# Performance work log

Measured on AMD Instinct MI355X. Metric: run time of the kernel, lower is better.

## Reference

```python
import jax, jax.numpy as jnp
import numpy as np

DIM = 128
EXPAND = 2
INTERNAL = DIM * EXPAND  # 256
MAX_SEQ = 2048
BATCH = 32
GATE_DECAY = 3.0


def _gated_cell(x, Wa, ba, Wi, bi, g):
    # x: [B,S,D]; Wa,Wi: [E,D]; ba,bi,g: [E]
    pa = jnp.einsum('bsd,ed->bse', x, Wa) + ba          # projected activation
    pi = jnp.einsum('bsd,ed->bse', x, Wi) + bi          # projected input
    reset_gate = jax.nn.sigmoid(pa)
    input_gate = jax.nn.sigmoid(pi)
    alpha = jax.nn.sigmoid(g)                           # [E]
    a = alpha / jnp.power(GATE_DECAY, reset_gate)       # adaptive alpha [B,S,E]
    u = jnp.sqrt(1.0 - a * a) * (input_gate * pi)       # per-step input [B,S,E]

    def step(h, au):
        a_t, u_t = au
        h = a_t * h + u_t
        return h, h

    h0 = jnp.zeros((x.shape[0], Wa.shape[0]), x.dtype)
    _, ys = jax.lax.scan(step, h0, (a.transpose(1, 0, 2), u.transpose(1, 0, 2)))
    return ys.transpose(1, 0, 2)                        # [B,S,E]


def _recency_weights(seq_len, dtype):
    w = jnp.exp(jnp.linspace(0.0, 3.0, MAX_SEQ))[:seq_len]
    return w.astype(dtype).reshape(1, -1, 1)


def setup_inputs() -> dict:
    key = jax.random.key(0)
    ks = jax.random.split(key, 12)
    std = 1.0 / np.sqrt(DIM)  # kaiming fan_in linear
    lo = float(np.log(0.9 / 0.1))
    hi = float(np.log(0.999 / 0.001))
    d = {
        'x': jax.random.normal(ks[0], (BATCH, MAX_SEQ, DIM), jnp.float32),
        'Wa_u': jax.random.normal(ks[1], (INTERNAL, DIM), jnp.float32) * std,
        'ba_u': jnp.zeros((INTERNAL,), jnp.float32),
        'Wi_u': jax.random.normal(ks[2], (INTERNAL, DIM), jnp.float32) * std,
        'bi_u': jnp.zeros((INTERNAL,), jnp.float32),
        'g_u': jax.random.uniform(ks[3], (INTERNAL,), jnp.float32, lo, hi),
        'Wa_w': jax.random.normal(ks[4], (INTERNAL, DIM), jnp.float32) * std,
        'ba_w': jnp.zeros((INTERNAL,), jnp.float32),
        'Wi_w': jax.random.normal(ks[5], (INTERNAL, DIM), jnp.float32) * std,
        'bi_w': jnp.zeros((INTERNAL,), jnp.float32),
        'g_w': jax.random.uniform(ks[6], (INTERNAL,), jnp.float32, lo, hi),
        'Wf': jax.random.normal(ks[7], (DIM, 4 * DIM), jnp.float32) * (1.0 / np.sqrt(4 * DIM)),
        'bf': jnp.zeros((DIM,), jnp.float32),
    }
    return d


def reference(x, Wa_u, ba_u, Wi_u, bi_u, g_u, Wa_w, ba_w, Wi_w, bi_w, g_w, Wf, bf):
    unweighted = _gated_cell(x, Wa_u, ba_u, Wi_u, bi_u, g_u)          # [B,S,2D]
    xw = x * _recency_weights(x.shape[1], x.dtype)
    weighted = _gated_cell(xw, Wa_w, ba_w, Wi_w, bi_w, g_w)           # [B,S,2D]
    combined = jnp.concatenate([unweighted, weighted], axis=-1)       # [B,S,4D]
    return jnp.einsum('bsf,df->bsd', combined, Wf) + bf               # [B,S,D]
```

## Files before the change

kernel.cpp:

```cpp
#include <hip/hip_runtime.h>
#include <hip/hip_fp16.h>
#include <cstddef>
#include <cstdint>

#define DIM 128
#define SEQ 2048
#define NB 32
#define NCH 512
#define NROWS (NB * SEQ)

typedef _Float16 half8 __attribute__((ext_vector_type(8)));
typedef float    f32x4 __attribute__((ext_vector_type(4)));

#define CMB_BYTES ((size_t)NROWS * NCH * 2)
#define WFG_OFF   CMB_BYTES
#define WFG_BYTES ((size_t)NCH * DIM * 2)
#define WS_NEEDED (WFG_OFF + WFG_BYTES)

__device__ __forceinline__ float sigf(float v) {
    return __builtin_amdgcn_rcpf(1.0f + __builtin_amdgcn_exp2f(v * -1.44269504f));
}

__device__ __forceinline__ half8 cvt8(float4 v0, float4 v1) {
    auto p0 = __builtin_amdgcn_cvt_pkrtz(v0.x, v0.y);
    auto p1 = __builtin_amdgcn_cvt_pkrtz(v0.z, v0.w);
    auto p2 = __builtin_amdgcn_cvt_pkrtz(v1.x, v1.y);
    auto p3 = __builtin_amdgcn_cvt_pkrtz(v1.z, v1.w);
    union U { half8 h8; decltype(p0) p[4]; } u;
    u.p[0] = p0; u.p[1] = p1; u.p[2] = p2; u.p[3] = p3;
    return u.h8;
}

__global__ void k0_wfg(const float* __restrict__ Wf, _Float16* __restrict__ Wfg) {
    int t = blockIdx.x * 256 + threadIdx.x;
#pragma unroll
    for (int i = 0; i < 8; ++i) {
        int o = t * 8 + i;
        int j    = o & 7;
        int lane = (o >> 3) & 63;
        int q    = lane >> 4, n16 = lane & 15;
        int ct   = (o >> 9) & 7;
        int ks   = (o >> 12) & 1;
        int kb   = o >> 13;
        int k = kb * 64 + ks * 32 + q * 8 + j;
        int n = ct * 16 + n16;
        Wfg[o] = (_Float16)Wf[n * NCH + k];
    }
}

__global__ __launch_bounds__(512, 2) void kfused(
        const float* __restrict__ x,
        const float* __restrict__ Wa_u, const float* __restrict__ ba_u,
        const float* __restrict__ Wi_u, const float* __restrict__ bi_u,
        const float* __restrict__ g_u,
        const float* __restrict__ Wa_w, const float* __restrict__ ba_w,
        const float* __restrict__ Wi_w, const float* __restrict__ bi_w,
        const float* __restrict__ g_w,
        _Float16* __restrict__ cmb) {
    __shared__ _Float16 Bs[8192];
    __shared__ float2   seg[32][33];
    __shared__ float    pref[32][33];
    __shared__ float    carry[32];

    const int tid  = threadIdx.x;
    const int lane = tid & 63;
    const int w    = tid >> 6;
    const int quad = lane >> 4;
    const int n16  = lane & 15;

    const int b  = blockIdx.x;
    const int cg = blockIdx.y;
    const int p  = cg >> 3;
    const int ebase = (cg & 7) * 32;

    const float* Wa  = p ? Wa_w : Wa_u;
    const float* Wi  = p ? Wi_w : Wi_u;
    const float* bap = p ? ba_w : ba_u;
    const float* bip = p ? bi_w : bi_u;
    const float* gp  = p ? g_w  : g_u;

    for (int sl = tid; sl < 1024; sl += 512) {
        int l  = sl & 63;
        int nt = (sl >> 6) & 3;
        int ks = sl >> 8;
        int qq = l >> 4, nn = l & 15;
        int e = ebase + (nt & 1) * 16 + nn;
        const float* Wp = (nt >> 1) ? Wi : Wa;
        const float* src = Wp + (size_t)e * DIM + ks * 32 + qq * 8;
        float4 v0 = *(const float4*)src;
        float4 v1 = *(const float4*)(src + 4);
        *(half8*)&Bs[sl * 8] = cvt8(v0, v1);
    }

    float rba[2], rbi[2], ral[2];
#pragma unroll
    for (int hh = 0; hh < 2; ++hh) {
        int e = ebase + hh * 16 + n16;
        rba[hh] = bap[e];
        rbi[hh] = bip[e];
        ral[hh] = sigf(gp[e]);
    }
    if (tid < 32) carry[tid] = 0.0f;

    float scb = __expf((float)(w * 16 + quad * 4) * (3.0f / 2047.0f));
    const float r1    = __expf(3.0f / 2047.0f);
    const float r2    = r1 * r1;
    const float r3    = r2 * r1;
    const float cs128 = __expf(128.0f * 3.0f / 2047.0f);

    const float* xbase = x + ((size_t)b * SEQ + (size_t)(w * 16 + n16)) * DIM + quad * 8;
    _Float16* cmbb = cmb + (size_t)b * SEQ * NCH + cg * 32 + n16;

    __syncthreads();

    half8 af[4];
    {
        float4 xf0[8];
#pragma unroll
        for (int ks = 0; ks < 4; ++ks) {
            xf0[2 * ks]     = *(const float4*)(xbase + ks * 32);
            xf0[2 * ks + 1] = *(const float4*)(xbase + ks * 32 + 4);
        }
#pragma unroll
        for (int ks = 0; ks < 4; ++ks)
            af[ks] = cvt8(xf0[2 * ks], xf0[2 * ks + 1]);
    }

    for (int t = 0; t < 16; ++t) {
        const int s0 = t * 128;

        f32x4 acc[4];
#pragma unroll
        for (int nt = 0; nt < 4; ++nt) acc[nt] = (f32x4){0.f, 0.f, 0.f, 0.f};
#pragma unroll
        for (int ks = 0; ks < 4; ++ks) {
            half8 a = af[ks];
#pragma unroll
            for (int nt = 0; nt < 4; ++nt) {
                half8 bb = *(const half8*)&Bs[(ks * 256 + nt * 64 + lane) * 8];
                acc[nt] = __builtin_amdgcn_mfma_f32_16x16x32_f16(a, bb, acc[nt], 0, 0, 0);
            }
        }

        float4 xf[8];
        {
            int tn = (t + 1) & 15;
            const float* ab = xbase + (size_t)tn * 128 * DIM;
#pragma unroll
            for (int ks = 0; ks < 4; ++ks) {
                xf[2 * ks]     = *(const float4*)(ab + ks * 32);
                xf[2 * ks + 1] = *(const float4*)(ab + ks * 32 + 4);
            }
        }

        float sc[4];
        if (p) { sc[0] = scb; sc[1] = scb * r1; sc[2] = scb * r2; sc[3] = scb * r3; }
        else   { sc[0] = sc[1] = sc[2] = sc[3] = 1.0f; }
        scb *= cs128;

        float a_s[2][4], u_s[2][4];
#pragma unroll
        for (int hh = 0; hh < 2; ++hh) {
            float A4 = 1.0f, U4 = 0.0f;
#pragma unroll
            for (int reg = 0; reg < 4; ++reg) {
                float pa = fmaf(acc[hh][reg],     sc[reg], rba[hh]);
                float pi = fmaf(acc[2 + hh][reg], sc[reg], rbi[hh]);
                float rst = sigf(pa);
                float ig  = sigf(pi);
                float a   = ral[hh] * __builtin_amdgcn_exp2f(-rst * 1.5849625007211562f);
                float m   = fmaxf(fmaf(-a, a, 1.0f), 0.0f);
                float u   = __builtin_amdgcn_sqrtf(m) * (ig * pi);
                a_s[hh][reg] = a; u_s[hh][reg] = u;
                A4 *= a;
                U4 = fmaf(a, U4, u);
            }
            seg[w * 4 + quad][hh * 16 + n16] = make_float2(A4, U4);
        }
        __syncthreads();

        if (tid < 32) {
            float H = carry[tid];
#pragma unroll
            for (int g = 0; g < 2; ++g) {
                float2 sv[16];
#pragma unroll
                for (int j = 0; j < 16; ++j)
                    sv[j] = seg[g * 16 + j][tid];
#pragma unroll
                for (int j = 0; j < 16; ++j) {
                    pref[g * 16 + j][tid] = H;
                    H = fmaf(sv[j].x, H, sv[j].y);
                }
            }
            carry[tid] = H;
        }
#pragma unroll
        for (int ks = 0; ks < 4; ++ks)
            af[ks] = cvt8(xf[2 * ks], xf[2 * ks + 1]);
        __builtin_amdgcn_sched_barrier(0);
        __syncthreads();

#pragma unroll
        for (int hh = 0; hh < 2; ++hh) {
            float h = pref[w * 4 + quad][hh * 16 + n16];
            _Float16* dst = cmbb + (size_t)(s0 + w * 16 + quad * 4) * NCH + hh * 16;
#pragma unroll
            for (int reg = 0; reg < 4; ++reg) {
                h = fmaf(a_s[hh][reg], h, u_s[hh][reg]);
                dst[(size_t)reg * NCH] = (_Float16)h;
            }
        }
    }
}

__global__ __launch_bounds__(256, 2) void k3_mfma(
        const _Float16* __restrict__ cmb, const _Float16* __restrict__ Wfg,
        const float* __restrict__ bfv, float* __restrict__ out) {
    __shared__ _Float16 As[16 * 512];
    __shared__ _Float16 Bs[16 * 512];

    const int tid  = threadIdx.x;
    const int lane = tid & 63;
    const int w    = tid >> 6;
    const int row0 = blockIdx.x * 128;
    const int q    = lane >> 4;
    const int nn   = lane & 15;

    f32x4 acc[2][8];
#pragma unroll
    for (int rt = 0; rt < 2; ++rt)
#pragma unroll
        for (int ct = 0; ct < 8; ++ct)
            acc[rt][ct] = (f32x4){0.0f, 0.0f, 0.0f, 0.0f};

    for (int kb = 0; kb < 8; ++kb) {
        const int kc = kb * 64;
#pragma unroll
        for (int i = 0; i < 4; ++i) {
            int f = tid + i * 256;
            int r = f >> 3, k8 = f & 7;
            uint4 v = *(const uint4*)(cmb + (size_t)(row0 + r) * NCH + kc + k8 * 8);
            int rt = r >> 4, m = r & 15, ks = k8 >> 2, qq = k8 & 3;
            *(uint4*)&As[(((rt * 2 + ks) * 64) + qq * 16 + m) * 8] = v;
        }
#pragma unroll
        for (int i = 0; i < 4; ++i) {
            int f = tid + i * 256;
            uint4 v = *(const uint4*)(Wfg + (size_t)kb * 8192 + (size_t)f * 8);
            *(uint4*)&Bs[(size_t)f * 8] = v;
        }
        __syncthreads();

#pragma unroll
        for (int ks = 0; ks < 2; ++ks) {
            half8 a0 = *(const half8*)&As[(((w * 2 + 0) * 2 + ks) * 512) + lane * 8];
            half8 a1 = *(const half8*)&As[(((w * 2 + 1) * 2 + ks) * 512) + lane * 8];
#pragma unroll
            for (int ct = 0; ct < 8; ++ct) {
                half8 bb = *(const half8*)&Bs[((ks * 8 + ct) * 512) + lane * 8];
                acc[0][ct] = __builtin_amdgcn_mfma_f32_16x16x32_f16(a0, bb, acc[0][ct], 0, 0, 0);
                acc[1][ct] = __builtin_amdgcn_mfma_f32_16x16x32_f16(a1, bb, acc[1][ct], 0, 0, 0);
            }
        }
        __syncthreads();
    }

#pragma unroll
    for (int rt = 0; rt < 2; ++rt) {
        int rbase = row0 + w * 32 + rt * 16 + q * 4;
#pragma unroll
        for (int ct = 0; ct < 8; ++ct) {
            int col = ct * 16 + nn;
            float bias = bfv[col];
#pragma unroll
            for (int reg = 0; reg < 4; ++reg)
                out[(size_t)(rbase + reg) * DIM + col] = acc[rt][ct][reg] + bias;
        }
    }
}

extern "C" void kernel_launch(void* const* d_in, const int* in_sizes, int n_in,
                              void* d_out, int out_size, void* d_ws, size_t ws_size,
                              hipStream_t stream) {
    if (ws_size < WS_NEEDED) return;

    const float* x    = (const float*)d_in[0];
    const float* Wa_u = (const float*)d_in[1];
    const float* ba_u = (const float*)d_in[2];
    const float* Wi_u = (const float*)d_in[3];
    const float* bi_u = (const float*)d_in[4];
    const float* g_u  = (const float*)d_in[5];
    const float* Wa_w = (const float*)d_in[6];
    const float* ba_w = (const float*)d_in[7];
    const float* Wi_w = (const float*)d_in[8];
    const float* bi_w = (const float*)d_in[9];
    const float* g_w  = (const float*)d_in[10];
    const float* Wf   = (const float*)d_in[11];
    const float* bfv  = (const float*)d_in[12];
    float* out = (float*)d_out;

    char* ws = (char*)d_ws;
    _Float16* cmb = (_Float16*)ws;
    _Float16* Wfg = (_Float16*)(ws + WFG_OFF);

    hipLaunchKernelGGL(k0_wfg, dim3(32), dim3(256), 0, stream, Wf, Wfg);
    hipLaunchKernelGGL(kfused, dim3(32, 16), dim3(512), 0, stream,
                       x, Wa_u, ba_u, Wi_u, bi_u, g_u,
                       Wa_w, ba_w, Wi_w, bi_w, g_w, cmb);
    hipLaunchKernelGGL(k3_mfma, dim3(512), dim3(256), 0, stream,
                       cmb, Wfg, bfv, out);
}
```

Measured before the change: 188.2 us.

## Store combined buffer in MFMA fragment layout, shuffle-based scan, async LDS double buffering

The fused scan kernel now writes the intermediate combined activations directly in the tiled fragment layout the output GEMM consumes. This lets the GEMM kernel stream tiles into LDS with global_load_lds and double buffering instead of scattered register loads. The cross-segment scan replaces the serial 32-thread prefix loop and its extra barrier with a wave-level shuffle scan plus a per-wave serial combine over the other waves. The LDS footprint of the GEMM doubles, which may lower occupancy, and the layout coupling between the two kernels is tight.

```diff
diff --git a/kernel.cpp b/kernel.cpp
--- a/kernel.cpp
+++ b/kernel.cpp
@@ -29,6 +29,13 @@
     union U { half8 h8; decltype(p0) p[4]; } u;
     u.p[0] = p0; u.p[1] = p1; u.p[2] = p2; u.p[3] = p3;
     return u.h8;
+}
+
+__device__ __forceinline__ void gload_lds16(const _Float16* g, _Float16* l) {
+    __builtin_amdgcn_global_load_lds(
+        (const __attribute__((address_space(1))) void*)g,
+        (__attribute__((address_space(3))) void*)l,
+        16, 0, 0);
 }
 
 __global__ void k0_wfg(const float* __restrict__ Wf, _Float16* __restrict__ Wfg) {
@@ -58,9 +65,8 @@
         const float* __restrict__ g_w,
         _Float16* __restrict__ cmb) {
     __shared__ _Float16 Bs[8192];
-    __shared__ float2   seg[32][33];
-    __shared__ float    pref[32][33];
-    __shared__ float    carry[32];
+    __shared__ float2   Wseg[2][8][33];
+    __shared__ float    carryL[2][32];
 
     const int tid  = threadIdx.x;
     const int lane = tid & 63;
@@ -100,7 +106,7 @@
         rbi[hh] = bip[e];
         ral[hh] = sigf(gp[e]);
     }
-    if (tid < 32) carry[tid] = 0.0f;
+    if (tid < 32) carryL[0][tid] = 0.0f;
 
     float scb = __expf((float)(w * 16 + quad * 4) * (3.0f / 2047.0f));
     const float r1    = __expf(3.0f / 2047.0f);
@@ -109,7 +115,9 @@
     const float cs128 = __expf(128.0f * 3.0f / 2047.0f);
 
     const float* xbase = x + ((size_t)b * SEQ + (size_t)(w * 16 + n16)) * DIM + quad * 8;
-    _Float16* cmbb = cmb + (size_t)b * SEQ * NCH + cg * 32 + n16;
+    _Float16* dst0 = cmb + (size_t)(cg >> 1) * 8192 + (size_t)w * 1024
+                   + (size_t)(cg & 1) * 512
+                   + (size_t)quad * 32 + (size_t)(n16 >> 3) * 128 + (n16 & 7);
 
     __syncthreads();
 
@@ -127,8 +135,6 @@
     }
 
     for (int t = 0; t < 16; ++t) {
-        const int s0 = t * 128;
-
         f32x4 acc[4];
 #pragma unroll
         for (int nt = 0; nt < 4; ++nt) acc[nt] = (f32x4){0.f, 0.f, 0.f, 0.f};
@@ -159,6 +165,7 @@
         scb *= cs128;
 
         float a_s[2][4], u_s[2][4];
+        float IA[2], IU[2], EA[2], EU[2];
 #pragma unroll
         for (int hh = 0; hh < 2; ++hh) {
             float A4 = 1.0f, U4 = 0.0f;
@@ -175,55 +182,67 @@
                 A4 *= a;
                 U4 = fmaf(a, U4, u);
             }
-            seg[w * 4 + quad][hh * 16 + n16] = make_float2(A4, U4);
-        }
+            float A = A4, U = U4;
+            float Ap = __shfl_up(A, 16); float Up = __shfl_up(U, 16);
+            bool c1 = quad >= 1;
+            U = c1 ? fmaf(A, Up, U) : U;
+            A = c1 ? A * Ap : A;
+            Ap = __shfl_up(A, 32); Up = __shfl_up(U, 32);
+            bool c2 = quad >= 2;
+            U = c2 ? fmaf(A, Up, U) : U;
+            A = c2 ? A * Ap : A;
+            IA[hh] = A; IU[hh] = U;
+            float Ae = __shfl_up(A, 16), Ue = __shfl_up(U, 16);
+            EA[hh] = (quad == 0) ? 1.0f : Ae;
+            EU[hh] = (quad == 0) ? 0.0f : Ue;
+        }
+        if (quad == 3) {
+#pragma unroll
+            for (int hh = 0; hh < 2; ++hh)
+                Wseg[t & 1][w][hh * 16 + n16] = make_float2(IA[hh], IU[hh]);
+        }
+
         __syncthreads();
 
-        if (tid < 32) {
-            float H = carry[tid];
-#pragma unroll
-            for (int g = 0; g < 2; ++g) {
-                float2 sv[16];
-#pragma unroll
-                for (int j = 0; j < 16; ++j)
-                    sv[j] = seg[g * 16 + j][tid];
-#pragma unroll
-                for (int j = 0; j < 16; ++j) {
-                    pref[g * 16 + j][tid] = H;
-                    H = fmaf(sv[j].x, H, sv[j].y);
-                }
-            }
-            carry[tid] = H;
-        }
 #pragma unroll
         for (int ks = 0; ks < 4; ++ks)
             af[ks] = cvt8(xf[2 * ks], xf[2 * ks + 1]);
-        __builtin_amdgcn_sched_barrier(0);
-        __syncthreads();
-
+
+        _Float16* dstT = dst0 + (size_t)((b * 16 + t) * 8) * 8192;
 #pragma unroll
         for (int hh = 0; hh < 2; ++hh) {
-            float h = pref[w * 4 + quad][hh * 16 + n16];
-            _Float16* dst = cmbb + (size_t)(s0 + w * 16 + quad * 4) * NCH + hh * 16;
+            int ch = hh * 16 + n16;
+            float h = carryL[t & 1][ch];
+#pragma unroll
+            for (int jj = 0; jj < 7; ++jj) {
+                if (jj < w) {
+                    float2 v = Wseg[t & 1][jj][ch];
+                    h = fmaf(v.x, h, v.y);
+                }
+            }
+            h = fmaf(EA[hh], h, EU[hh]);
 #pragma unroll
             for (int reg = 0; reg < 4; ++reg) {
                 h = fmaf(a_s[hh][reg], h, u_s[hh][reg]);
-                dst[(size_t)reg * NCH] = (_Float16)h;
-            }
+                dstT[hh * 256 + reg * 8] = (_Float16)h;
+            }
+            if (w == 7 && quad == 3)
+                carryL[(t + 1) & 1][ch] = h;
         }
     }
 }
 
 __global__ __launch_bounds__(256, 2) void k3_mfma(
-        const _Float16* __restrict__ cmb, const _Float16* __restrict__ Wfg,
+        const _Float16* __restrict__ cmbF, const _Float16* __restrict__ Wfg,
         const float* __restrict__ bfv, float* __restrict__ out) {
-    __shared__ _Float16 As[16 * 512];
-    __shared__ _Float16 Bs[16 * 512];
+    __shared__ _Float16 As[2][8192];
+    __shared__ _Float16 Bs[2][8192];
 
     const int tid  = threadIdx.x;
     const int lane = tid & 63;
     const int w    = tid >> 6;
-    const int row0 = blockIdx.x * 128;
+    const int rb   = blockIdx.x;
+    const int row0 = rb * 128;
     const int q    = lane >> 4;
     const int nn   = lane & 15;
 
@@ -234,31 +253,35 @@
         for (int ct = 0; ct < 8; ++ct)
             acc[rt][ct] = (f32x4){0.0f, 0.0f, 0.0f, 0.0f};
 
+#define K3_STAGE(buf, kb)                                                     \
+    {                                                                         \
+        const _Float16* sa = cmbF + ((size_t)rb * 8 + (kb)) * 8192            \
+                           + (size_t)w * 2048 + (size_t)lane * 8;             \
+        const _Float16* sb = Wfg + (size_t)(kb) * 8192                        \
+                           + (size_t)w * 2048 + (size_t)lane * 8;             \
+        _Float16* la = &As[buf][w * 2048];                                    \
+        _Float16* lb = &Bs[buf][w * 2048];                                    \
+        _Pragma("unroll")                                                     \
+        for (int i = 0; i < 4; ++i) {                                         \
+            gload_lds16(sa + i * 512, la + i * 512);                          \
+            gload_lds16(sb + i * 512, lb + i * 512);                          \
+        }                                                                     \
+    }
+
+    K3_STAGE(0, 0);
+    __syncthreads();
+
     for (int kb = 0; kb < 8; ++kb) {
-        const int kc = kb * 64;
-#pragma unroll
-        for (int i = 0; i < 4; ++i) {
-            int f = tid + i * 256;
-            int r = f >> 3, k8 = f & 7;
-            uint4 v = *(const uint4*)(cmb + (size_t)(row0 + r) * NCH + kc + k8 * 8);
-            int rt = r >> 4, m = r & 15, ks = k8 >> 2, qq = k8 & 3;
-            *(uint4*)&As[(((rt * 2 + ks) * 64) + qq * 16 + m) * 8] = v;
-        }
-#pragma unroll
-        for (int i = 0; i < 4; ++i) {
-            int f = tid + i * 256;
-            uint4 v = *(const uint4*)(Wfg + (size_t)kb * 8192 + (size_t)f * 8);
-            *(uint4*)&Bs[(size_t)f * 8] = v;
-        }
-        __syncthreads();
+        const int cur = kb & 1;
+        if (kb < 7) K3_STAGE(cur ^ 1, kb + 1);
 
 #pragma unroll
         for (int ks = 0; ks < 2; ++ks) {
-            half8 a0 = *(const half8*)&As[(((w * 2 + 0) * 2 + ks) * 512) + lane * 8];
-            half8 a1 = *(const half8*)&As[(((w * 2 + 1) * 2 + ks) * 512) + lane * 8];
+            half8 a0 = *(const half8*)&As[cur][(((w * 2 + 0) * 2 + ks) * 512) + lane * 8];
+            half8 a1 = *(const half8*)&As[cur][(((w * 2 + 1) * 2 + ks) * 512) + lane * 8];
 #pragma unroll
             for (int ct = 0; ct < 8; ++ct) {
-                half8 bb = *(const half8*)&Bs[((ks * 8 + ct) * 512) + lane * 8];
+                half8 bb = *(const half8*)&Bs[cur][((ks * 8 + ct) * 512) + lane * 8];
                 acc[0][ct] = __builtin_amdgcn_mfma_f32_16x16x32_f16(a0, bb, acc[0][ct], 0, 0, 0);
                 acc[1][ct] = __builtin_amdgcn_mfma_f32_16x16x32_f16(a1, bb, acc[1][ct], 0, 0, 0);
             }
@@ -278,6 +301,7 @@
                 out[(size_t)(rbase + reg) * DIM + col] = acc[rt][ct][reg] + bias;
         }
     }
+#undef K3_STAGE
 }
 
 extern "C" void kernel_launch(void* const* d_in, const int* in_sizes, int n_in,
```

Result: no change. 189.4 us (+0.7%).
